# Kernel tuning notes

Measured on AMD Instinct MI355X. Metric: run time of the kernel, lower is better.

Reference implementation:

```python
import jax, jax.numpy as jnp
import numpy as np

DIM = 1024
NUM_HEADS = 16
HEAD_DIM = DIM // NUM_HEADS
SCALE = HEAD_DIM ** -0.5


def setup_inputs() -> dict:
    key = jax.random.key(0)
    k1, k2, k3 = jax.random.split(key, 3)
    x = jax.random.normal(k1, (4, 2048, DIM), dtype=jnp.float32)
    w_qkv = jax.random.normal(k2, (DIM, 3 * DIM), dtype=jnp.float32) * (DIM ** -0.5)
    b_qkv = jnp.zeros((3 * DIM,), dtype=jnp.float32)
    w_proj = jax.random.normal(k3, (DIM, DIM), dtype=jnp.float32) * (DIM ** -0.5)
    b_proj = jnp.zeros((DIM,), dtype=jnp.float32)
    return {"x": x, "w_qkv": w_qkv, "b_qkv": b_qkv, "w_proj": w_proj, "b_proj": b_proj}


def reference(x, w_qkv, b_qkv, w_proj, b_proj):
    b, n, c = x.shape
    qkv = x @ w_qkv + b_qkv                       # [b, n, 3*dim]
    qkv = qkv.reshape(b, n, 3, NUM_HEADS, HEAD_DIM)
    qkv = jnp.transpose(qkv, (2, 0, 3, 1, 4))     # [3, b, H, n, hd]
    q, k, v = qkv[0], qkv[1], qkv[2]
    attn = jnp.einsum("bhqd,bhkd->bhqk", q, k) * SCALE
    attn = jax.nn.softmax(attn, axis=-1)
    out = jnp.einsum("bhqk,bhkd->bhqd", attn, v)  # [b, H, n, hd]
    out = jnp.transpose(out, (0, 2, 1, 3)).reshape(b, n, c)
    return out @ w_proj + b_proj
```

## Files before the change

kernel.cpp:

```cpp
#include <hip/hip_runtime.h>
#include <hip/hip_bf16.h>

typedef unsigned short u16;
typedef __attribute__((ext_vector_type(8))) short bf16x8;
typedef __attribute__((ext_vector_type(4))) float f32x4;
typedef __attribute__((ext_vector_type(16))) float f32x16;


__device__ __forceinline__ u16 f2bf(float f) {
  union { float f; unsigned u; } v; v.f = f;
  unsigned r = v.u + 0x7fffu + ((v.u >> 16) & 1u);
  return (u16)(r >> 16);
}

#if defined(__has_builtin)
#if __has_builtin(__builtin_amdgcn_cvt_pk_bf16_f32)
#define HAS_PK_BF16 1
#endif
#endif
__device__ __forceinline__ unsigned pk2bf(float a, float b) {
#ifdef HAS_PK_BF16
  typedef __attribute__((ext_vector_type(2))) __bf16 vbf2;
  union { vbf2 v; unsigned u; } u;
  u.v = __builtin_amdgcn_cvt_pk_bf16_f32(a, b);
  return u.u;
#else
  return (unsigned)f2bf(a) | ((unsigned)f2bf(b) << 16);
#endif
}

__device__ __forceinline__ f32x4 mfma16(bf16x8 a, bf16x8 b, f32x4 c) {
  return __builtin_amdgcn_mfma_f32_16x16x32_bf16(a, b, c, 0, 0, 0);
}
__device__ __forceinline__ f32x16 mfma32(bf16x8 a, bf16x8 b, f32x16 c) {
  return __builtin_amdgcn_mfma_f32_32x32x16_bf16(a, b, c, 0, 0, 0);
}

__device__ __forceinline__ void gl_lds16(const void* g, void* l) {
  __builtin_amdgcn_global_load_lds((__attribute__((address_space(1))) void*)g,
                                   (__attribute__((address_space(3))) void*)l,
                                   16, 0, 0);
}


__global__ void cvt_f32_bf16(const float* __restrict__ in, u16* __restrict__ out, int n) {
  int i = (blockIdx.x * blockDim.x + threadIdx.x) * 4;
  if (i >= n) return;
  float4 v = *(const float4*)(in + i);
  u16 o0 = f2bf(v.x), o1 = f2bf(v.y), o2 = f2bf(v.z), o3 = f2bf(v.w);
  ushort4 o; o.x = o0; o.y = o1; o.z = o2; o.w = o3;
  *(ushort4*)(out + i) = o;
}

__global__ void transpose_cvt2(const float* __restrict__ wq, const float* __restrict__ wp,
                               u16* __restrict__ oq, u16* __restrict__ op) {
  __shared__ u16 tile[64][65];
  const int bx = blockIdx.x;
  const float* in; u16* out; int C, c0;
  if (bx < 48) { in = wq; out = oq; C = 3072; c0 = bx * 64; }
  else         { in = wp; out = op; C = 1024; c0 = (bx - 48) * 64; }
  const int R = 1024;
  int r0 = blockIdx.y * 64;
  int lc = threadIdx.x & 63, lr = threadIdx.x >> 6;
#pragma unroll
  for (int i = 0; i < 16; ++i) {
    int r = lr + i * 4;
    tile[r][lc] = f2bf(in[(size_t)(r0 + r) * C + c0 + lc]);
  }
  __syncthreads();
#pragma unroll
  for (int i = 0; i < 16; ++i) {
    int c = lr + i * 4;
    out[(size_t)(c0 + c) * R + r0 + lc] = tile[lc][c];
  }
}


struct Smem128 { u16 A0[8192]; u16 B0[16384]; u16 A1[8192]; u16 B1[16384]; };

#define LDB128(base, off) (*(const bf16x8*)((const char*)(base) + (off)))
#define ISSUE_A(dst, j, k0) \
  gl_lds16(pA + (size_t)(j) * 32768 + (k0), (dst) + (j) * 4096 + dsel)
#define ISSUE_B(dst, j, k0) \
  gl_lds16(pB + (size_t)(j) * 65536 + (k0), (dst) + (j) * 4096 + dsel)

#define KSTEP(CA, CB, NA, NB, k0n, PF)                                         \
  do {                                                                         \
    bf16x8 aL[2][2], aH[2][2], bL[2][2], bH[2][2];                             \
            \
    _Pragma("unroll") for (int mt = 0; mt < 2; ++mt) {                         \
      aL[mt][0] = LDB128(CA, aoff + mt * 2048 + cp0);                          \
      aL[mt][1] = LDB128(CA, aoff + mt * 2048 + cp1);                          \
    }                                                                          \
    _Pragma("unroll") for (int nt = 0; nt < 2; ++nt) {                         \
      bL[nt][0] = LDB128(CB, boff + nt * 2048 + cp0);                          \
      bL[nt][1] = LDB128(CB, boff + nt * 2048 + cp1);                          \
    }                                                                          \
    if (PF) { ISSUE_B(NB, 0, k0n); ISSUE_B(NB, 1, k0n); }                      \
    __builtin_amdgcn_s_setprio(1);                                             \
    _Pragma("unroll") for (int mt = 0; mt < 2; ++mt)                           \
      _Pragma("unroll") for (int nt = 0; nt < 2; ++nt) {                       \
        acc[mt][nt] = mfma16(aL[mt][0], bL[nt][0], acc[mt][nt]);               \
        acc[mt][nt] = mfma16(aL[mt][1], bL[nt][1], acc[mt][nt]);               \
      }                                                                        \
    __builtin_amdgcn_s_setprio(0);                                             \
                             \
    _Pragma("unroll") for (int nt = 0; nt < 2; ++nt) {                         \
      bH[nt][0] = LDB128(CB, boff + (nt + 2) * 2048 + cp0);                    \
      bH[nt][1] = LDB128(CB, boff + (nt + 2) * 2048 + cp1);                    \
    }                                                                          \
    if (PF) { ISSUE_B(NB, 2, k0n); ISSUE_B(NB, 3, k0n); }                      \
    __builtin_amdgcn_s_setprio(1);                                             \
    _Pragma("unroll") for (int mt = 0; mt < 2; ++mt)                           \
      _Pragma("unroll") for (int nt = 0; nt < 2; ++nt) {                       \
        acc[mt][nt + 2] = mfma16(aL[mt][0], bH[nt][0], acc[mt][nt + 2]);       \
        acc[mt][nt + 2] = mfma16(aL[mt][1], bH[nt][1], acc[mt][nt + 2]);       \
      }                                                                        \
    __builtin_amdgcn_s_setprio(0);                                             \
       \
    if (PF) asm volatile("s_waitcnt vmcnt(4)" ::: "memory");                   \
    else    asm volatile("s_waitcnt vmcnt(0)" ::: "memory");                   \
    __builtin_amdgcn_s_barrier();                                              \
    _Pragma("unroll") for (int mt = 0; mt < 2; ++mt) {                         \
      aH[mt][0] = LDB128(CA, 8192 + aoff + mt * 2048 + cp0);                   \
      aH[mt][1] = LDB128(CA, 8192 + aoff + mt * 2048 + cp1);                   \
    }                                                                          \
    if (PF) ISSUE_A(NA, 0, k0n);                                               \
    __builtin_amdgcn_s_setprio(1);                                             \
    _Pragma("unroll") for (int mt = 0; mt < 2; ++mt)                           \
      _Pragma("unroll") for (int nt = 0; nt < 2; ++nt) {                       \
        acc[mt + 2][nt + 2] = mfma16(aH[mt][0], bH[nt][0], acc[mt + 2][nt + 2]); \
        acc[mt + 2][nt + 2] = mfma16(aH[mt][1], bH[nt][1], acc[mt + 2][nt + 2]); \
      }                                                                        \
    __builtin_amdgcn_s_setprio(0);                                             \
                   \
    if (PF) ISSUE_A(NA, 1, k0n);                                               \
    __builtin_amdgcn_s_setprio(1);                                             \
    _Pragma("unroll") for (int mt = 0; mt < 2; ++mt)                           \
      _Pragma("unroll") for (int nt = 0; nt < 2; ++nt) {                       \
        acc[mt + 2][nt] = mfma16(aH[mt][0], bL[nt][0], acc[mt + 2][nt]);       \
        acc[mt + 2][nt] = mfma16(aH[mt][1], bL[nt][1], acc[mt + 2][nt]);       \
      }                                                                        \
    __builtin_amdgcn_s_setprio(0);                                             \
    if (PF) asm volatile("s_waitcnt vmcnt(1)" ::: "memory");                   \
    __builtin_amdgcn_s_barrier();                                              \
  } while (0)

#define GEMM128_SETUP(Amat, Bmat)                                              \
  __shared__ Smem128 sm;                                                       \
  const int t = threadIdx.x, lane = t & 63, wave = t >> 6;                     \
  const int quad = lane >> 4, l15 = lane & 15;                                 \
  const int wm = wave >> 2, wn = wave & 3;                                     \
  const int row0 = blockIdx.x * 128, col0 = blockIdx.y * 256;                  \
  const int g = t >> 3, f0 = g + (g & 32);      \
  const int swz = (t & 7) ^ (g & 7);                                           \
  const u16* pA = (Amat) + (size_t)(row0 + f0) * 1024 + swz * 8;               \
  const u16* pB = (Bmat) + (size_t)(col0 + g) * 1024 + swz * 8;                \
  const size_t dsel = (size_t)wave * 512;                                      \
  const int rm = l15 & 7;                                                      \
  const int aoff = wm * 4096 + l15 * 128;                                      \
  const int boff = (wn * 64 + l15) * 128;                                      \
  const int cp0 = (quad ^ rm) << 4, cp1 = ((quad + 4) ^ rm) << 4;              \
  f32x4 acc[4][4] = {};                                                        \
  ISSUE_B(sm.B0, 0, 0); ISSUE_B(sm.B0, 1, 0);                                  \
  ISSUE_B(sm.B0, 2, 0); ISSUE_B(sm.B0, 3, 0);                                  \
  ISSUE_A(sm.A0, 0, 0); ISSUE_A(sm.A0, 1, 0);                                  \
  asm volatile("s_waitcnt vmcnt(1)" ::: "memory");                             \
  __builtin_amdgcn_s_barrier();                                                \
  _Pragma("unroll 1")                                                          \
  for (int kk = 0; kk < 8; ++kk) {                                             \
    KSTEP(sm.A0, sm.B0, sm.A1, sm.B1, (2 * kk + 1) * 64, 1);                   \
    KSTEP(sm.A1, sm.B1, sm.A0, sm.B0, (2 * kk + 2) * 64, (kk < 7));            \
  }


__global__ __launch_bounds__(512, 2) void gemm_qkv(
    const u16* __restrict__ A, const u16* __restrict__ Bt,
    const float* __restrict__ bias,
    u16* __restrict__ Qb, u16* __restrict__ Kb, u16* __restrict__ Vt) {
  GEMM128_SETUP(A, Bt)

  const int which = col0 >> 10;

  if (which == 2) {
    u16* Ts = ((u16*)&sm) + wave * 4096;
#pragma unroll
    for (int nt = 0; nt < 4; ++nt) {
      const int d = nt * 16 + l15;
      const float bv = bias[col0 + wn * 64 + nt * 16 + l15];
#pragma unroll
      for (int mt = 0; mt < 4; ++mt) {
        uint2 pk;
        pk.x = pk2bf(acc[mt][nt][0] + bv, acc[mt][nt][1] + bv);
        pk.y = pk2bf(acc[mt][nt][2] + bv, acc[mt][nt][3] + bv);
        *(uint2*)((char*)Ts + d * 128 +
                  (((mt * 4 + quad) ^ ((d & 7) << 1)) << 3)) = pk;
      }
    }
    const int h = ((col0 - 2048) >> 6) + wn;
    const int b_ = row0 >> 11;
    const int s0w = (row0 & 2047) + wm * 64;
    u16* vt = Vt + (size_t)(b_ * 16 + h) * 64 * 2048;
#pragma unroll
    for (int i = 0; i < 8; ++i) {
      const int d = i * 8 + (lane >> 3), c = lane & 7;
      uint4 v = *(const uint4*)((const char*)Ts + d * 128 + ((c ^ (d & 7)) << 4));
      *(uint4*)(vt + (size_t)d * 2048 + s0w + c * 8) = v;
    }
    return;
  }

  u16* dst = which == 0 ? Qb : Kb;
  const float qscale = which == 0 ? 0.1803368801111137f : 1.0f;
#pragma unroll
  for (int nt = 0; nt < 4; ++nt) {
    const int col = (col0 & 1023) + wn * 64 + nt * 16 + l15;
    const float bv = bias[col0 + wn * 64 + nt * 16 + l15];
    const int h = col >> 6, d = col & 63;
#pragma unroll
    for (int mt = 0; mt < 4; ++mt) {
#pragma unroll
      for (int r = 0; r < 4; ++r) {
        const int row = row0 + wm * 64 + mt * 16 + quad * 4 + r;
        const int bb = row >> 11, s = row & 2047;
        dst[(((size_t)bb * 16 + h) * 2048 + s) * 64 + d] =
            f2bf((acc[mt][nt][r] + bv) * qscale);
      }
    }
  }
}


__global__ __launch_bounds__(512, 2) void gemm_proj(
    const u16* __restrict__ A, const u16* __restrict__ Bt,
    const float* __restrict__ bias, float* __restrict__ C) {
  GEMM128_SETUP(A, Bt)

#pragma unroll
  for (int nt = 0; nt < 4; ++nt) {
    const int col = col0 + wn * 64 + nt * 16 + l15;
    const float bv = bias[col];
#pragma unroll
    for (int mt = 0; mt < 4; ++mt) {
#pragma unroll
      for (int r = 0; r < 4; ++r) {
        const int row = row0 + wm * 64 + mt * 16 + quad * 4 + r;
        C[(size_t)row * 1024 + col] = acc[mt][nt][r] + bv;
      }
    }
  }
}


__device__ __forceinline__ void softmax32(const f32x16& s, float& l,
                                          bf16x8& paA, bf16x8& paB) {
  unsigned D[8];
#pragma unroll
  for (int i = 0; i < 8; ++i) {
    float a = __builtin_amdgcn_exp2f(s[2 * i]);
    float b = __builtin_amdgcn_exp2f(s[2 * i + 1]);
    l += a + b;
    D[i] = pk2bf(a, b);
  }
  {
    unsigned x = D[0], x2 = D[1], y = D[2], y2 = D[3];
    asm volatile("v_permlane32_swap_b32 %0, %1" : "+v"(x), "+v"(y));
    asm volatile("v_permlane32_swap_b32 %0, %1" : "+v"(x2), "+v"(y2));
    union { unsigned u[4]; bf16x8 v; } p;
    p.u[0] = x; p.u[1] = x2; p.u[2] = y; p.u[3] = y2;
    paA = p.v;
  }
  {
    unsigned x = D[4], x2 = D[5], y = D[6], y2 = D[7];
    asm volatile("v_permlane32_swap_b32 %0, %1" : "+v"(x), "+v"(y));
    asm volatile("v_permlane32_swap_b32 %0, %1" : "+v"(x2), "+v"(y2));
    union { unsigned u[4]; bf16x8 v; } p;
    p.u[0] = x; p.u[1] = x2; p.u[2] = y; p.u[3] = y2;
    paB = p.v;
  }
}

__global__ __launch_bounds__(256, 2) void attn_kernel(
    const u16* __restrict__ Qb, const u16* __restrict__ Kb,
    const u16* __restrict__ Vt, u16* __restrict__ Ob) {
  __shared__ u16 KsA[64 * 64], KsB[64 * 64];
  __shared__ u16 VsA[64 * 64], VsB[64 * 64];
  const int bh = blockIdx.x, q0 = blockIdx.y * 256;
  const u16* Qp = Qb + (size_t)bh * 2048 * 64;
  const u16* Kp = Kb + (size_t)bh * 2048 * 64;
  const u16* Vp = Vt + (size_t)bh * 64 * 2048;
  const int t = threadIdx.x, lane = t & 63, wave = t >> 6;
  const int l31 = lane & 31, hi = lane >> 5;

  const int kr0 = t >> 3, kc0 = (t & 7) ^ (kr0 & 7);
  const int kr1 = (256 + t) >> 3, kc1 = ((256 + t) & 7) ^ (kr1 & 7);
  const u16* Kg0 = Kp + (size_t)kr0 * 64 + kc0 * 8;
  const u16* Kg1 = Kp + (size_t)kr1 * 64 + kc1 * 8;
  const u16* Vg0 = Vp + (size_t)kr0 * 2048 + kc0 * 8;
  const u16* Vg1 = Vp + (size_t)kr1 * 2048 + kc1 * 8;
  const size_t dof0 = (size_t)wave * 512;
  const size_t dof1 = 2048 + (size_t)wave * 512;

#define STAGE(Kd, Vd, key0)                                   \
  do {                                                        \
    gl_lds16(Kg0 + (size_t)(key0) * 64, (Kd) + dof0);         \
    gl_lds16(Kg1 + (size_t)(key0) * 64, (Kd) + dof1);         \
    gl_lds16(Vg0 + (key0), (Vd) + dof0);                      \
    gl_lds16(Vg1 + (key0), (Vd) + dof1);                      \
  } while (0)

  STAGE(KsA, VsA, 0);
  const u16* Qr0 = Qp + (size_t)(q0 + wave * 64 + l31) * 64 + hi * 8;
  const u16* Qr1 = Qr0 + 32 * 64;
  bf16x8 qf0[4], qf1[4];
#pragma unroll
  for (int dc = 0; dc < 4; ++dc) {
    qf0[dc] = *(const bf16x8*)(Qr0 + dc * 16);
    qf1[dc] = *(const bf16x8*)(Qr1 + dc * 16);
  }
  __syncthreads();

  const int rm = l31 & 7;
  int off[2][4];
#pragma unroll
  for (int x = 0; x < 2; ++x)
#pragma unroll
    for (int c = 0; c < 4; ++c)
      off[x][c] = x * 4096 + l31 * 128 + (((c * 2 + hi) ^ rm) << 4);

  f32x16 acc00 = {}, acc01 = {}, acc10 = {}, acc11 = {};
  float l0 = 0.f, l1 = 0.f;

#define TILE(Ks, Vs)                                                          \
  do {                                                                        \
    _Pragma("unroll")                                                         \
    for (int kh = 0; kh < 2; ++kh) {                                          \
      f32x16 s0 = {}, s1 = {};                                                \
      __builtin_amdgcn_s_setprio(1);                                          \
      _Pragma("unroll")                                                       \
      for (int dc = 0; dc < 4; ++dc) {                                        \
        bf16x8 kf = *(const bf16x8*)((const char*)(Ks) + off[kh][dc]);        \
        s0 = mfma32(kf, qf0[dc], s0);                                         \
        s1 = mfma32(kf, qf1[dc], s1);                                         \
      }                                                                       \
      __builtin_amdgcn_s_setprio(0);                                          \
      bf16x8 pa00, pa01, pa10, pa11;                                          \
      softmax32(s0, l0, pa00, pa01);                                          \
      softmax32(s1, l1, pa10, pa11);                                          \
      __builtin_amdgcn_s_setprio(1);                                          \
      _Pragma("unroll")                                                       \
      for (int ci = 0; ci < 2; ++ci) {                                        \
        const int c = 2 * kh + ci;                                            \
        bf16x8 vlo = *(const bf16x8*)((const char*)(Vs) + off[0][c]);         \
        bf16x8 vhiv = *(const bf16x8*)((const char*)(Vs) + off[1][c]);        \
        bf16x8 pa0 = ci ? pa01 : pa00;                                        \
        bf16x8 pa1 = ci ? pa11 : pa10;                                        \
        acc00 = mfma32(pa0, vlo, acc00);                                      \
        acc01 = mfma32(pa0, vhiv, acc01);                                     \
        acc10 = mfma32(pa1, vlo, acc10);                                      \
        acc11 = mfma32(pa1, vhiv, acc11);                                     \
      }                                                                       \
      __builtin_amdgcn_s_setprio(0);                                          \
    }                                                                         \
  } while (0)

#pragma unroll 1
  for (int kt2 = 0; kt2 < 16; ++kt2) {
    const int kt = kt2 * 2;
    STAGE(KsB, VsB, (kt + 1) * 64);
    TILE(KsA, VsA);
    __syncthreads();
    if (kt2 < 15) STAGE(KsA, VsA, (kt + 2) * 64);
    TILE(KsB, VsB);
    __syncthreads();
  }
#undef TILE
#undef STAGE

  l0 += __shfl_xor(l0, 32);
  l1 += __shfl_xor(l1, 32);
  float inv0 = 1.f / l0, inv1 = 1.f / l1;

  const int b_ = bh >> 4, h = bh & 15;
  const int qw = q0 + wave * 64;
#pragma unroll
  for (int r = 0; r < 16; ++r) {
    const int ql = (r & 3) + 8 * (r >> 2) + 4 * hi;
    float iv0 = __shfl(inv0, ql);
    float iv1 = __shfl(inv1, ql);
    size_t base0 = ((size_t)b_ * 2048 + qw + ql) * 1024 + h * 64;
    size_t base1 = base0 + (size_t)32 * 1024;
    Ob[base0 + l31] = f2bf(acc00[r] * iv0);
    Ob[base0 + 32 + l31] = f2bf(acc01[r] * iv0);
    Ob[base1 + l31] = f2bf(acc10[r] * iv1);
    Ob[base1 + 32 + l31] = f2bf(acc11[r] * iv1);
  }
}


extern "C" void kernel_launch(void* const* d_in, const int* in_sizes, int n_in,
                              void* d_out, int out_size, void* d_ws, size_t ws_size,
                              hipStream_t stream) {
  const float* x      = (const float*)d_in[0];
  const float* w_qkv  = (const float*)d_in[1];
  const float* b_qkv  = (const float*)d_in[2];
  const float* w_proj = (const float*)d_in[3];
  const float* b_proj = (const float*)d_in[4];
  float* out = (float*)d_out;
  char* ws = (char*)d_ws;

  u16* xb    = (u16*)(ws);
  u16* wqkvt = (u16*)(ws + 16777216);
  u16* wprjt = (u16*)(ws + 23068672);
  u16* Qb    = (u16*)(ws + 25165824);
  u16* Kb    = (u16*)(ws + 41943040);
  u16* Vt    = (u16*)(ws + 58720256);
  u16* Ob    = xb;
  if (ws_size < 92274688u) return;

  cvt_f32_bf16<<<8192, 256, 0, stream>>>(x, xb, 8388608);
  transpose_cvt2<<<dim3(64, 16), 256, 0, stream>>>(w_qkv, w_proj, wqkvt, wprjt);
  gemm_qkv<<<dim3(64, 12), 512, 0, stream>>>(xb, wqkvt, b_qkv, Qb, Kb, Vt);
  attn_kernel<<<dim3(64, 8), 256, 0, stream>>>(Qb, Kb, Vt, Ob);
  gemm_proj<<<dim3(64, 4), 512, 0, stream>>>(Ob, wprjt, b_proj, out);
}
```

Measured before the change: 255.9 us.

## Fuse input prep kernels, remap GEMM block order, batch attention QK over full tile

Merges the x conversion and the weight transpose-convert into one prep launch, which saves a kernel launch and gap. GEMM blocks now use a 1D grid with a swizzled mapping, so consecutive blocks in each group of 64 spread over row tiles, which may change L2 reuse. The attention tile now computes all four QK score blocks before running softmax and PV, instead of two half passes. That exposes more independent MFMAs at the cost of more live registers.

```diff
diff --git a/kernel.cpp b/kernel.cpp
--- a/kernel.cpp
+++ b/kernel.cpp
@@ -43,25 +43,26 @@
 }
 
 
-__global__ void cvt_f32_bf16(const float* __restrict__ in, u16* __restrict__ out, int n) {
-  int i = (blockIdx.x * blockDim.x + threadIdx.x) * 4;
-  if (i >= n) return;
-  float4 v = *(const float4*)(in + i);
-  u16 o0 = f2bf(v.x), o1 = f2bf(v.y), o2 = f2bf(v.z), o3 = f2bf(v.w);
-  ushort4 o; o.x = o0; o.y = o1; o.z = o2; o.w = o3;
-  *(ushort4*)(out + i) = o;
-}
-
-__global__ void transpose_cvt2(const float* __restrict__ wq, const float* __restrict__ wp,
-                               u16* __restrict__ oq, u16* __restrict__ op) {
+__global__ void prep(const float* __restrict__ x, const float* __restrict__ wq,
+                     const float* __restrict__ wp, u16* __restrict__ xb,
+                     u16* __restrict__ oq, u16* __restrict__ op) {
   __shared__ u16 tile[64][65];
-  const int bx = blockIdx.x;
+  const int b = blockIdx.x, t = threadIdx.x;
+  if (b < 8192) {
+    int i = (b * 256 + t) * 4;
+    float4 v = *(const float4*)(x + i);
+    ushort4 o;
+    o.x = f2bf(v.x); o.y = f2bf(v.y); o.z = f2bf(v.z); o.w = f2bf(v.w);
+    *(ushort4*)(xb + i) = o;
+    return;
+  }
+  const int tb = b - 8192;
+  const int bx = tb & 63, by = tb >> 6;
   const float* in; u16* out; int C, c0;
   if (bx < 48) { in = wq; out = oq; C = 3072; c0 = bx * 64; }
   else         { in = wp; out = op; C = 1024; c0 = (bx - 48) * 64; }
-  const int R = 1024;
-  int r0 = blockIdx.y * 64;
-  int lc = threadIdx.x & 63, lr = threadIdx.x >> 6;
+  const int R = 1024, r0 = by * 64;
+  const int lc = t & 63, lr = t >> 6;
 #pragma unroll
   for (int i = 0; i < 16; ++i) {
     int r = lr + i * 4;
@@ -151,7 +152,9 @@
   const int t = threadIdx.x, lane = t & 63, wave = t >> 6;                     \
   const int quad = lane >> 4, l15 = lane & 15;                                 \
   const int wm = wave >> 2, wn = wave & 3;                                     \
-  const int row0 = blockIdx.x * 128, col0 = blockIdx.y * 256;                  \
+  const int bid = blockIdx.x;                                                  \
+  const int bx = (bid & 7) * 8 + ((bid >> 3) & 7);    \
+  const int row0 = bx * 128, col0 = (bid >> 6) * 256;                          \
   const int g = t >> 3, f0 = g + (g & 32);      \
   const int swz = (t & 7) ^ (g & 7);                                           \
   const u16* pA = (Amat) + (size_t)(row0 + f0) * 1024 + swz * 8;               \
@@ -333,35 +336,37 @@
 
 #define TILE(Ks, Vs)                                                          \
   do {                                                                        \
+    f32x16 s00 = {}, s01 = {}, s10 = {}, s11 = {};              \
+    __builtin_amdgcn_s_setprio(1);                                            \
     _Pragma("unroll")                                                         \
-    for (int kh = 0; kh < 2; ++kh) {                                          \
-      f32x16 s0 = {}, s1 = {};                                                \
-      __builtin_amdgcn_s_setprio(1);                                          \
-      _Pragma("unroll")                                                       \
-      for (int dc = 0; dc < 4; ++dc) {                                        \
-        bf16x8 kf = *(const bf16x8*)((const char*)(Ks) + off[kh][dc]);        \
-        s0 = mfma32(kf, qf0[dc], s0);                                         \
-        s1 = mfma32(kf, qf1[dc], s1);                                         \
-      }                                                                       \
-      __builtin_amdgcn_s_setprio(0);                                          \
-      bf16x8 pa00, pa01, pa10, pa11;                                          \
-      softmax32(s0, l0, pa00, pa01);                                          \
-      softmax32(s1, l1, pa10, pa11);                                          \
-      __builtin_amdgcn_s_setprio(1);                                          \
+    for (int dc = 0; dc < 4; ++dc) {                                          \
+      bf16x8 kf0 = *(const bf16x8*)((const char*)(Ks) + off[0][dc]);          \
+      bf16x8 kf1 = *(const bf16x8*)((const char*)(Ks) + off[1][dc]);          \
+      s00 = mfma32(kf0, qf0[dc], s00);                                        \
+      s01 = mfma32(kf0, qf1[dc], s01);                                        \
+      s10 = mfma32(kf1, qf0[dc], s10);                                        \
+      s11 = mfma32(kf1, qf1[dc], s11);                                        \
+    }                                                                         \
+    __builtin_amdgcn_s_setprio(0);                                            \
+    bf16x8 pa[2][2][2];                                  \
+    softmax32(s00, l0, pa[0][0][0], pa[0][0][1]);                             \
+    softmax32(s01, l1, pa[0][1][0], pa[0][1][1]);                             \
+    softmax32(s10, l0, pa[1][0][0], pa[1][0][1]);                             \
+    softmax32(s11, l1, pa[1][1][0], pa[1][1][1]);                             \
+    __builtin_amdgcn_s_setprio(1);                                            \
+    _Pragma("unroll")                                                         \
+    for (int kh = 0; kh < 2; ++kh)                                            \
       _Pragma("unroll")                                                       \
       for (int ci = 0; ci < 2; ++ci) {                                        \
         const int c = 2 * kh + ci;                                            \
         bf16x8 vlo = *(const bf16x8*)((const char*)(Vs) + off[0][c]);         \
-        bf16x8 vhiv = *(const bf16x8*)((const char*)(Vs) + off[1][c]);        \
-        bf16x8 pa0 = ci ? pa01 : pa00;                                        \
-        bf16x8 pa1 = ci ? pa11 : pa10;                                        \
-        acc00 = mfma32(pa0, vlo, acc00);                                      \
-        acc01 = mfma32(pa0, vhiv, acc01);                                     \
-        acc10 = mfma32(pa1, vlo, acc10);                                      \
-        acc11 = mfma32(pa1, vhiv, acc11);                                     \
+        bf16x8 vhi2 = *(const bf16x8*)((const char*)(Vs) + off[1][c]);        \
+        acc00 = mfma32(pa[kh][0][ci], vlo, acc00);                            \
+        acc01 = mfma32(pa[kh][0][ci], vhi2, acc01);                           \
+        acc10 = mfma32(pa[kh][1][ci], vlo, acc10);                            \
+        acc11 = mfma32(pa[kh][1][ci], vhi2, acc11);                           \
       }                                                                       \
-      __builtin_amdgcn_s_setprio(0);                                          \
-    }                                                                         \
+    __builtin_amdgcn_s_setprio(0);                                            \
   } while (0)
 
 #pragma unroll 1
@@ -418,9 +423,8 @@
   u16* Ob    = xb;
   if (ws_size < 92274688u) return;
 
-  cvt_f32_bf16<<<8192, 256, 0, stream>>>(x, xb, 8388608);
-  transpose_cvt2<<<dim3(64, 16), 256, 0, stream>>>(w_qkv, w_proj, wqkvt, wprjt);
-  gemm_qkv<<<dim3(64, 12), 512, 0, stream>>>(xb, wqkvt, b_qkv, Qb, Kb, Vt);
+  prep<<<9216, 256, 0, stream>>>(x, w_qkv, w_proj, xb, wqkvt, wprjt);
+  gemm_qkv<<<768, 512, 0, stream>>>(xb, wqkvt, b_qkv, Qb, Kb, Vt);
   attn_kernel<<<dim3(64, 8), 256, 0, stream>>>(Qb, Kb, Vt, Ob);
-  gemm_proj<<<dim3(64, 4), 512, 0, stream>>>(Ob, wprjt, b_proj, out);
-}
+  gemm_proj<<<256, 512, 0, stream>>>(Ob, wprjt, b_proj, out);
+}
```

Result: slower. 277.4 us (+8.4%).
